# Performance work log

Measured on AMD Instinct MI355X. Metric: run time of the kernel, lower is better.

## Reference

```python
import jax, jax.numpy as jnp
import numpy as np

WS = 8          # window size
NH = 16         # num heads
C = 256         # in_channels
L = WS * WS     # tokens per window
EPS = 1e-5      # LayerNorm eps

def _rel_index():
    coords = np.stack(np.meshgrid(np.arange(WS), np.arange(WS), indexing='ij')).reshape(2, -1)
    rel = coords[:, :, None] - coords[:, None, :]
    rel = rel + (WS - 1)
    rel[0] = rel[0] * (2 * WS - 1)
    return jnp.asarray(rel.sum(0))  # [L, L] int

REL_IDX = _rel_index()

def _ln(x, g, b):
    m = x.mean(-1, keepdims=True)
    v = jnp.var(x, axis=-1, keepdims=True)
    return (x - m) * jax.lax.rsqrt(v + EPS) * g + b

def setup_inputs() -> dict:
    key = jax.random.key(0)
    ks = jax.random.split(key, 8)
    return {
        'x': jax.random.normal(ks[0], (2, C, 256, 256), dtype=jnp.float32),
        'pre_gamma': jnp.ones((C,), jnp.float32),
        'pre_beta': jnp.zeros((C,), jnp.float32),
        'post_gamma': jnp.ones((C,), jnp.float32),
        'post_beta': jnp.zeros((C,), jnp.float32),
        'qkv_w': jax.random.normal(ks[1], (C, 3 * C), jnp.float32) * 0.02,
        'qkv_b': jnp.zeros((3 * C,), jnp.float32),
        'proj_w': jax.random.normal(ks[2], (C, C), jnp.float32) * 0.02,
        'proj_b': jnp.zeros((C,), jnp.float32),
        'rel_bias_table': jax.random.normal(ks[3], ((2 * WS - 1) ** 2, NH), jnp.float32) * 0.02,
    }

def reference(x, pre_gamma, pre_beta, post_gamma, post_beta, qkv_w, qkv_b, proj_w, proj_b, rel_bias_table):
    N, Cc, H, W = x.shape
    # block partition: [N,C,H,W] -> [N*nWin, L, C]
    t = x.reshape(N, Cc, H // WS, WS, W // WS, WS)
    t = t.transpose(0, 2, 4, 3, 5, 1).reshape(-1, L, Cc)
    B = t.shape[0]
    # pre-norm + relative self-attention (cosine / normalized qk)
    y = _ln(t, pre_gamma, pre_beta)
    qkv = (y @ qkv_w + qkv_b).reshape(B, L, 3, NH, Cc // NH).transpose(2, 0, 3, 1, 4)
    q, k, v = qkv[0], qkv[1], qkv[2]  # [B, h, L, dh]
    q = q / jnp.maximum(jnp.linalg.norm(q, axis=-1, keepdims=True), 1e-12)
    k = k / jnp.maximum(jnp.linalg.norm(k, axis=-1, keepdims=True), 1e-12)
    bias = rel_bias_table[REL_IDX].transpose(2, 0, 1)  # [h, L, L]
    attn = jax.nn.softmax(jnp.einsum('bhld,bhmd->bhlm', q, k) + bias, axis=-1)
    o = jnp.einsum('bhlm,bhmd->bhld', attn, v).transpose(0, 2, 1, 3).reshape(B, L, Cc)
    o = o @ proj_w + proj_b
    out = t + o
    # post-norm residual (mlp is Identity in MetNet-3)
    out = out + _ln(out, post_gamma, post_beta)
    # reverse partition -> [N, C, H, W]
    out = out.reshape(N, H // WS, W // WS, WS, WS, Cc)
    out = out.transpose(0, 5, 1, 3, 2, 4).reshape(N, Cc, H, W)
    return out
```

## Files before the change

kernel.cpp:

```cpp
#include <hip/hip_runtime.h>


#define WSZ 8
#define LTOK 64
#define NH 16
#define CCH 256
#define WW2 256
#define HWP 65536
#define NWIN 2048

#define TP 258
#define QP2 18
#define VP2 66
#define PP2 66
#define OHP 36

typedef __bf16 bf16x8 __attribute__((ext_vector_type(8)));
typedef float  f32x4  __attribute__((ext_vector_type(4)));
typedef unsigned short u16;
typedef unsigned long long ull;
typedef uint4  __attribute__((may_alias)) uint4_a;
typedef float4 __attribute__((may_alias)) float4_a;
typedef ull    __attribute__((may_alias)) ull_a;

__device__ __forceinline__ float b2f(u16 u) {
    return (float)__builtin_bit_cast(__bf16, u);
}
__device__ __forceinline__ u16 f2b(float f) {
    return __builtin_bit_cast(u16, (__bf16)f);
}
__device__ __forceinline__ __bf16 u2b(u16 u) {
    return __builtin_bit_cast(__bf16, u);
}
__device__ __forceinline__ float gload(const void* p, int idx, int isf32) {
    return isf32 ? ((const float*)p)[idx] : b2f(((const u16*)p)[idx]);
}

static __global__ void detect_dtype(const u16* __restrict__ xu, int* __restrict__ flag) {
    int lane = threadIdx.x;
    u16 u = xu[lane];
    int e = (u >> 7) & 0xFF;
    bool plaus = (u == 0) || (e >= 0x6C && e <= 0x86);
    unsigned long long m = __ballot(plaus);
    if (lane == 0) flag[0] = (__popcll(m) >= 56) ? 0 : 1;
}

static __global__ __launch_bounds__(256) void prep_qkv(
        const void* __restrict__ qkv_w, const void* __restrict__ qkv_b,
        const void* __restrict__ g, const void* __restrict__ be,
        u16* __restrict__ gwT, float* __restrict__ D2, float* __restrict__ D3,
        const int* __restrict__ flagp)
{
    const int isf32 = flagp[0];
    int col0 = blockIdx.x * 4;
    int c    = threadIdx.x;
    float gv = gload(g, c, isf32), bv = gload(be, c, isf32);
    float w4[4];
    if (isf32) {
        float4 w = *(const float4_a*)((const float*)qkv_w + c * 768 + col0);
        w4[0] = w.x; w4[1] = w.y; w4[2] = w.z; w4[3] = w.w;
    } else {
        ull u = *(const ull_a*)((const u16*)qkv_w + c * 768 + col0);
        w4[0] = b2f((u16)u);         w4[1] = b2f((u16)(u >> 16));
        w4[2] = b2f((u16)(u >> 32)); w4[3] = b2f((u16)(u >> 48));
    }
    float s2[4], s3[4];
    #pragma unroll
    for (int j = 0; j < 4; ++j) {
        float gw = gv * w4[j];
        gwT[(col0 + j) * 256 + c] = f2b(gw);
        s2[j] = gw; s3[j] = bv * w4[j];
    }
    #pragma unroll
    for (int off = 32; off; off >>= 1) {
        #pragma unroll
        for (int j = 0; j < 4; ++j) {
            s2[j] += __shfl_xor(s2[j], off);
            s3[j] += __shfl_xor(s3[j], off);
        }
    }
    __shared__ float p2[4][4], p3[4][4];
    int wvid = threadIdx.x >> 6, ln = threadIdx.x & 63;
    if (ln == 0) {
        #pragma unroll
        for (int j = 0; j < 4; ++j) { p2[wvid][j] = s2[j]; p3[wvid][j] = s3[j]; }
    }
    __syncthreads();
    if (threadIdx.x < 4) {
        int j = threadIdx.x;
        D2[col0 + j] = p2[0][j] + p2[1][j] + p2[2][j] + p2[3][j];
        D3[col0 + j] = p3[0][j] + p3[1][j] + p3[2][j] + p3[3][j]
                     + gload(qkv_b, col0 + j, isf32);
    }
}

static __global__ __launch_bounds__(256) void prep_proj(
        const void* __restrict__ proj_w, u16* __restrict__ pwT,
        const void* __restrict__ table, float* __restrict__ tablef,
        const int* __restrict__ flagp)
{
    const int isf32 = flagp[0];
    int n0 = blockIdx.x * 4, k = threadIdx.x;
    float w4[4];
    if (isf32) {
        float4 w = *(const float4_a*)((const float*)proj_w + k * 256 + n0);
        w4[0] = w.x; w4[1] = w.y; w4[2] = w.z; w4[3] = w.w;
    } else {
        ull u = *(const ull_a*)((const u16*)proj_w + k * 256 + n0);
        w4[0] = b2f((u16)u);         w4[1] = b2f((u16)(u >> 16));
        w4[2] = b2f((u16)(u >> 32)); w4[3] = b2f((u16)(u >> 48));
    }
    #pragma unroll
    for (int j = 0; j < 4; ++j) pwT[(n0 + j) * 256 + k] = f2b(w4[j]);
    int gid = blockIdx.x * 256 + threadIdx.x;
    if (gid < (2 * WSZ - 1) * (2 * WSZ - 1) * NH)
        tablef[gid] = gload(table, gid, isf32);
}

static __global__ __launch_bounds__(256, 3) void win_attn(
    const void* __restrict__ x, void* __restrict__ out,
    const u16* __restrict__ gwT, const u16* __restrict__ pwT,
    const float* __restrict__ D2, const float* __restrict__ D3,
    const void* __restrict__ proj_b, const void* __restrict__ postg,
    const void* __restrict__ postb, const float* __restrict__ tablef,
    const int* __restrict__ flagp)
{
    __shared__ __align__(16) u16 smu[19968];
    u16* const sm_t  = smu;
    u16* const sm_qb = smu;
    u16* const sm_kb = smu + 4608;
    u16* const sm_vb = smu + 9216;
    u16* const sm_pb = smu + 13440;
    u16* const sm_ob = smu + 17664;
    __shared__ float sm_mean[LTOK], sm_rstd[LTOK];
    __shared__ u16 sm_zero[16];

    const int isf32 = flagp[0];
    const int tid  = threadIdx.x;
    const int wv   = tid >> 6;
    const int lane = tid & 63;
    const int quad = lane >> 4;
    const int n15  = lane & 15;

    const int b  = blockIdx.x;
    const int nb = b >> 10, wh = (b >> 5) & 31, wwi = b & 31;
    const int base = nb * (CCH * HWP) + wh * (8 * WW2) + wwi * 8;

    if (tid < 16) sm_zero[tid] = 0;

    if (isf32) {
        const float* xf = (const float*)x;
        #pragma unroll
        for (int r = 0; r < 8; ++r) {
            int s = tid + r * 256;
            int c = s >> 3, i = s & 7;
            const float* src = xf + base + c * HWP + i * WW2;
            float4 a = *(const float4_a*)(src);
            float4 d = *(const float4_a*)(src + 4);
            u16* dst = &sm_t[(i * 8) * TP + c];
            dst[0 * TP] = f2b(a.x);  dst[1 * TP] = f2b(a.y);
            dst[2 * TP] = f2b(a.z);  dst[3 * TP] = f2b(a.w);
            dst[4 * TP] = f2b(d.x);  dst[5 * TP] = f2b(d.y);
            dst[6 * TP] = f2b(d.z);  dst[7 * TP] = f2b(d.w);
        }
    } else {
        const u16* xu = (const u16*)x;
        #pragma unroll
        for (int r = 0; r < 8; ++r) {
            int s = tid + r * 256;
            int c = s >> 3, i = s & 7;
            const uint4 v = *(const uint4_a*)(xu + base + c * HWP + i * WW2);
            u16* dst = &sm_t[(i * 8) * TP + c];
            dst[0 * TP] = (u16)(v.x & 0xffff);  dst[1 * TP] = (u16)(v.x >> 16);
            dst[2 * TP] = (u16)(v.y & 0xffff);  dst[3 * TP] = (u16)(v.y >> 16);
            dst[4 * TP] = (u16)(v.z & 0xffff);  dst[5 * TP] = (u16)(v.z >> 16);
            dst[6 * TP] = (u16)(v.w & 0xffff);  dst[7 * TP] = (u16)(v.w >> 16);
        }
    }
    __syncthreads();

    {
        int l = tid >> 2, g = tid & 3;
        float s = 0.f, ss = 0.f;
        const u16* row = &sm_t[l * TP + g * 64];
        #pragma unroll
        for (int e = 0; e < 64; ++e) {
            float a = b2f(row[e]);
            s += a; ss += a * a;
        }
        s += __shfl_xor(s, 1); ss += __shfl_xor(ss, 1);
        s += __shfl_xor(s, 2); ss += __shfl_xor(ss, 2);
        if (g == 0) {
            float mean = s * (1.f / 256.f);
            float var  = ss * (1.f / 256.f) - mean * mean;
            sm_mean[l] = mean;
            sm_rstd[l] = rsqrtf(var + 1e-5f);
        }
    }

    float s4[4], ms4[4];
    #pragma unroll
    for (int r = 0; r < 4; ++r) {
        int tok = wv * 16 + quad * 4 + r;
        float mu = sm_mean[tok], sd = sm_rstd[tok];
        s4[r] = sd; ms4[r] = -mu * sd;
    }

    bf16x8 afr[8];
    {
        const u16* arow = &sm_t[(wv * 16 + n15) * TP];
        #pragma unroll
        for (int kb = 0; kb < 8; ++kb) {
            #pragma unroll
            for (int j = 0; j < 8; ++j)
                afr[kb][j] = u2b(arow[kb * 32 + quad * 8 + j]);
        }
    }
    __syncthreads();

    int toff[4][4];
    #pragma unroll
    for (int ct = 0; ct < 4; ++ct) {
        int key = ct * 16 + n15, im = key >> 3, jm = key & 7;
        #pragma unroll
        for (int r = 0; r < 4; ++r) {
            int tok = wv * 16 + quad * 4 + r;
            int il = tok >> 3, jl = tok & 7;
            toff[ct][r] = ((il - im + 7) * 15 + (jl - jm + 7)) * 16;
        }
    }

    f32x4 accp[16];
    #pragma unroll
    for (int t2 = 0; t2 < 16; ++t2) accp[t2] = f32x4{0.f, 0.f, 0.f, 0.f};
    const f32x4 zero4 = f32x4{0.f, 0.f, 0.f, 0.f};

    bf16x8 onesf;
    #pragma unroll
    for (int j = 0; j < 8; ++j) onesf[j] = (__bf16)1.0f;

    for (int hq = 0; hq < 4; ++hq) {
        const int H = hq * 4;

        f32x4 aq[4], ak[4], av[4];
        #pragma unroll
        for (int hh = 0; hh < 4; ++hh) { aq[hh] = zero4; ak[hh] = zero4; av[hh] = zero4; }
        const u16* g0 = &gwT[(H * 16 + n15) * 256 + quad * 8];
        #pragma unroll
        for (int kb = 0; kb < 8; ++kb) {
            #pragma unroll
            for (int hh = 0; hh < 4; ++hh) {
                const u16* gq = g0 + hh * 4096 + kb * 32;
                bf16x8 bq = __builtin_bit_cast(bf16x8, *(const uint4_a*)(gq));
                bf16x8 bk = __builtin_bit_cast(bf16x8, *(const uint4_a*)(gq + 65536));
                bf16x8 bv = __builtin_bit_cast(bf16x8, *(const uint4_a*)(gq + 131072));
                aq[hh] = __builtin_amdgcn_mfma_f32_16x16x32_bf16(afr[kb], bq, aq[hh], 0, 0, 0);
                ak[hh] = __builtin_amdgcn_mfma_f32_16x16x32_bf16(afr[kb], bk, ak[hh], 0, 0, 0);
                av[hh] = __builtin_amdgcn_mfma_f32_16x16x32_bf16(afr[kb], bv, av[hh], 0, 0, 0);
            }
        }
        #pragma unroll
        for (int hh = 0; hh < 4; ++hh) {
            int ci = (H + hh) * 16 + n15;
            float d2q = D2[ci],       d3q = D3[ci];
            float d2k = D2[256 + ci], d3k = D3[256 + ci];
            float d2v = D2[512 + ci], d3v = D3[512 + ci];
            float qv[4], kv[4], vv[4];
            #pragma unroll
            for (int r = 0; r < 4; ++r) {
                qv[r] = s4[r] * aq[hh][r] + ms4[r] * d2q + d3q;
                kv[r] = s4[r] * ak[hh][r] + ms4[r] * d2k + d3k;
                vv[r] = s4[r] * av[hh][r] + ms4[r] * d2v + d3v;
            }
            #pragma unroll
            for (int r = 0; r < 4; ++r) {
                float sq = qv[r] * qv[r], sk = kv[r] * kv[r];
                sq += __shfl_xor(sq, 1); sk += __shfl_xor(sk, 1);
                sq += __shfl_xor(sq, 2); sk += __shfl_xor(sk, 2);
                sq += __shfl_xor(sq, 4); sk += __shfl_xor(sk, 4);
                sq += __shfl_xor(sq, 8); sk += __shfl_xor(sk, 8);
                qv[r] *= rsqrtf(fmaxf(sq, 1e-24f));
                kv[r] *= rsqrtf(fmaxf(sk, 1e-24f));
            }
            #pragma unroll
            for (int r = 0; r < 4; ++r) {
                int tok = wv * 16 + quad * 4 + r;
                sm_qb[hh * 1152 + tok * QP2 + n15] = f2b(qv[r]);
                sm_kb[hh * 1152 + tok * QP2 + n15] = f2b(kv[r]);
                sm_vb[hh * 1056 + n15 * VP2 + tok] = f2b(vv[r]);
            }
        }
        __syncthreads();

        #pragma unroll
        for (int hh = 0; hh < 4; ++hh) {
            const int h = H + hh;
            f32x4 sc[4];
            {
                bf16x8 aqf;
                const u16* qrow = (quad < 2)
                    ? &sm_qb[hh * 1152 + (wv * 16 + n15) * QP2 + quad * 8]
                    : sm_zero;
                #pragma unroll
                for (int j = 0; j < 8; ++j) aqf[j] = u2b(qrow[j]);
                #pragma unroll
                for (int ct = 0; ct < 4; ++ct) {
                    bf16x8 bkf;
                    const u16* krow = (quad < 2)
                        ? &sm_kb[hh * 1152 + (ct * 16 + n15) * QP2 + quad * 8]
                        : sm_zero;
                    #pragma unroll
                    for (int j = 0; j < 8; ++j) bkf[j] = u2b(krow[j]);
                    f32x4 bias;
                    #pragma unroll
                    for (int r = 0; r < 4; ++r) bias[r] = tablef[toff[ct][r] + h];
                    sc[ct] = __builtin_amdgcn_mfma_f32_16x16x32_bf16(aqf, bkf, bias, 0, 0, 0);
                }
            }
            #pragma unroll
            for (int r = 0; r < 4; ++r) {
                float e0 = __expf(sc[0][r]), e1 = __expf(sc[1][r]);
                float e2 = __expf(sc[2][r]), e3 = __expf(sc[3][r]);
                int tok = wv * 16 + quad * 4 + r;
                sm_pb[tok * PP2 +  0 + n15] = f2b(e0);
                sm_pb[tok * PP2 + 16 + n15] = f2b(e1);
                sm_pb[tok * PP2 + 32 + n15] = f2b(e2);
                sm_pb[tok * PP2 + 48 + n15] = f2b(e3);
            }

            f32x4 ov = zero4, rs = zero4;
            #pragma unroll
            for (int ks = 0; ks < 2; ++ks) {
                bf16x8 ap, bvf;
                const u16* prow = &sm_pb[(wv * 16 + n15) * PP2 + ks * 32 + quad * 8];
                const u16* vrow = &sm_vb[hh * 1056 + n15 * VP2 + ks * 32 + quad * 8];
                #pragma unroll
                for (int j = 0; j < 8; ++j) { ap[j] = u2b(prow[j]); bvf[j] = u2b(vrow[j]); }
                ov = __builtin_amdgcn_mfma_f32_16x16x32_bf16(ap, bvf, ov, 0, 0, 0);
                rs = __builtin_amdgcn_mfma_f32_16x16x32_bf16(ap, onesf, rs, 0, 0, 0);
            }
            #pragma unroll
            for (int r = 0; r < 4; ++r) {
                int tok = wv * 16 + quad * 4 + r;
                sm_ob[tok * OHP + (h & 1) * 16 + n15] = f2b(ov[r] / rs[r]);
            }

            if (hh & 1) {
                int hp = h >> 1;
                bf16x8 aof;
                const u16* orow = &sm_ob[(wv * 16 + n15) * OHP + quad * 8];
                #pragma unroll
                for (int j = 0; j < 8; ++j) aof[j] = u2b(orow[j]);
                const u16* pwb = &pwT[n15 * 256 + hp * 32 + quad * 8];
                #pragma unroll
                for (int t2 = 0; t2 < 16; ++t2) {
                    bf16x8 bpf = __builtin_bit_cast(bf16x8, *(const uint4_a*)(pwb + t2 * 16 * 256));
                    accp[t2] = __builtin_amdgcn_mfma_f32_16x16x32_bf16(aof, bpf, accp[t2], 0, 0, 0);
                }
            }
        }
        __syncthreads();
    }

    if (isf32) {
        const float* xf = (const float*)x;
        #pragma unroll
        for (int r = 0; r < 8; ++r) {
            int s = tid + r * 256;
            int c = s >> 3, i = s & 7;
            const float* src = xf + base + c * HWP + i * WW2;
            float4 a = *(const float4_a*)(src);
            float4 d = *(const float4_a*)(src + 4);
            u16* dst = &sm_t[(i * 8) * TP + c];
            dst[0 * TP] = f2b(a.x);  dst[1 * TP] = f2b(a.y);
            dst[2 * TP] = f2b(a.z);  dst[3 * TP] = f2b(a.w);
            dst[4 * TP] = f2b(d.x);  dst[5 * TP] = f2b(d.y);
            dst[6 * TP] = f2b(d.z);  dst[7 * TP] = f2b(d.w);
        }
    } else {
        const u16* xu = (const u16*)x;
        #pragma unroll
        for (int r = 0; r < 8; ++r) {
            int s = tid + r * 256;
            int c = s >> 3, i = s & 7;
            const uint4 v = *(const uint4_a*)(xu + base + c * HWP + i * WW2);
            u16* dst = &sm_t[(i * 8) * TP + c];
            dst[0 * TP] = (u16)(v.x & 0xffff);  dst[1 * TP] = (u16)(v.x >> 16);
            dst[2 * TP] = (u16)(v.y & 0xffff);  dst[3 * TP] = (u16)(v.y >> 16);
            dst[4 * TP] = (u16)(v.z & 0xffff);  dst[5 * TP] = (u16)(v.z >> 16);
            dst[6 * TP] = (u16)(v.w & 0xffff);  dst[7 * TP] = (u16)(v.w >> 16);
        }
    }
    __syncthreads();

    {
        #pragma unroll
        for (int t2 = 0; t2 < 16; ++t2) {
            int col = t2 * 16 + n15;
            float pb = gload(proj_b, col, isf32);
            #pragma unroll
            for (int r = 0; r < 4; ++r) {
                int tok = wv * 16 + quad * 4 + r;
                accp[t2][r] += pb + b2f(sm_t[tok * TP + col]);
            }
        }
        float sr[4] = {0, 0, 0, 0}, ssr[4] = {0, 0, 0, 0};
        #pragma unroll
        for (int t2 = 0; t2 < 16; ++t2) {
            #pragma unroll
            for (int r = 0; r < 4; ++r) { float v = accp[t2][r]; sr[r] += v; ssr[r] += v * v; }
        }
        #pragma unroll
        for (int r = 0; r < 4; ++r) {
            sr[r] += __shfl_xor(sr[r], 1); ssr[r] += __shfl_xor(ssr[r], 1);
            sr[r] += __shfl_xor(sr[r], 2); ssr[r] += __shfl_xor(ssr[r], 2);
            sr[r] += __shfl_xor(sr[r], 4); ssr[r] += __shfl_xor(ssr[r], 4);
            sr[r] += __shfl_xor(sr[r], 8); ssr[r] += __shfl_xor(ssr[r], 8);
        }
        float mean2[4], rs2[4];
        #pragma unroll
        for (int r = 0; r < 4; ++r) {
            float m = sr[r] * (1.f / 256.f);
            float v = ssr[r] * (1.f / 256.f) - m * m;
            mean2[r] = m; rs2[r] = rsqrtf(v + 1e-5f);
        }
        #pragma unroll
        for (int t2 = 0; t2 < 16; ++t2) {
            int col = t2 * 16 + n15;
            float pg = gload(postg, col, isf32), pb2 = gload(postb, col, isf32);
            #pragma unroll
            for (int r = 0; r < 4; ++r) {
                int tok = wv * 16 + quad * 4 + r;
                float o1 = accp[t2][r];
                float fin = o1 + (o1 - mean2[r]) * rs2[r] * pg + pb2;
                sm_t[tok * TP + col] = f2b(fin);
            }
        }
    }
    __syncthreads();

    if (isf32) {
        float* outf = (float*)out;
        #pragma unroll
        for (int r = 0; r < 8; ++r) {
            int s = tid + r * 256;
            int c = s >> 3, i = s & 7;
            const u16* src = &sm_t[(i * 8) * TP + c];
            float* dst = outf + base + c * HWP + i * WW2;
            float4 a, d;
            a.x = b2f(src[0 * TP]); a.y = b2f(src[1 * TP]);
            a.z = b2f(src[2 * TP]); a.w = b2f(src[3 * TP]);
            d.x = b2f(src[4 * TP]); d.y = b2f(src[5 * TP]);
            d.z = b2f(src[6 * TP]); d.w = b2f(src[7 * TP]);
            *(float4_a*)dst = a;
            *(float4_a*)(dst + 4) = d;
        }
    } else {
        u16* outu = (u16*)out;
        #pragma unroll
        for (int r = 0; r < 8; ++r) {
            int s = tid + r * 256;
            int c = s >> 3, i = s & 7;
            const u16* src = &sm_t[(i * 8) * TP + c];
            uint4 v;
            v.x = (unsigned)src[0 * TP] | ((unsigned)src[1 * TP] << 16);
            v.y = (unsigned)src[2 * TP] | ((unsigned)src[3 * TP] << 16);
            v.z = (unsigned)src[4 * TP] | ((unsigned)src[5 * TP] << 16);
            v.w = (unsigned)src[6 * TP] | ((unsigned)src[7 * TP] << 16);
            *(uint4_a*)(outu + base + c * HWP + i * WW2) = v;
        }
    }
}

extern "C" void kernel_launch(void* const* d_in, const int* in_sizes, int n_in,
                              void* d_out, int out_size, void* d_ws, size_t ws_size,
                              hipStream_t stream) {
    const void* x     = d_in[0];
    const void* preg  = d_in[1];
    const void* preb  = d_in[2];
    const void* postg = d_in[3];
    const void* postb = d_in[4];
    const void* qkvw  = d_in[5];
    const void* qkvb  = d_in[6];
    const void* projw = d_in[7];
    const void* projb = d_in[8];
    const void* table = d_in[9];

    char* ws = (char*)d_ws;
    u16*   gwT = (u16*)(ws);
    u16*   pwT = (u16*)(ws + 393216);
    float* D2  = (float*)(ws + 524288);
    float* D3  = (float*)(ws + 527360);
    float* tbf = (float*)(ws + 530432);
    int*   flg = (int*)(ws + 544832);

    detect_dtype<<<1, 64, 0, stream>>>((const u16*)x, flg);
    prep_qkv<<<192, 256, 0, stream>>>(qkvw, qkvb, preg, preb, gwT, D2, D3, flg);
    prep_proj<<<64, 256, 0, stream>>>(projw, pwT, table, tbf, flg);
    win_attn<<<NWIN, 256, 0, stream>>>(x, d_out, gwT, pwT, D2, D3,
                                       projb, postg, postb, tbf, flg);
}
```

Before: 1.186 ms.

## Process four windows per block with dedicated LDS buffers to skip x reload

Each block now loops over four adjacent windows, so the grid shrinks from 2048 to 512 blocks. The shared-memory regions for the input tile, q, k, v, probabilities and head outputs no longer alias each other. Because the input tile stays resident, the residual add reads it from LDS instead of reloading x from global memory. The cost is much more LDS per block, launch bounds lowered from 3 to 2 blocks per CU, and windows processed serially inside a block, which reduces occupancy and latency hiding.

```diff
diff --git a/kernel.cpp b/kernel.cpp
--- a/kernel.cpp
+++ b/kernel.cpp
@@ -7,7 +7,7 @@
 #define CCH 256
 #define WW2 256
 #define HWP 65536
-#define NWIN 2048
+#define NBLK 512
 
 #define TP 258
 #define QP2 18
@@ -117,7 +117,7 @@
         tablef[gid] = gload(table, gid, isf32);
 }
 
-static __global__ __launch_bounds__(256, 3) void win_attn(
+static __global__ __launch_bounds__(256, 2) void win_attn(
     const void* __restrict__ x, void* __restrict__ out,
     const u16* __restrict__ gwT, const u16* __restrict__ pwT,
     const float* __restrict__ D2, const float* __restrict__ D3,
@@ -125,13 +125,12 @@
     const void* __restrict__ postb, const float* __restrict__ tablef,
     const int* __restrict__ flagp)
 {
-    __shared__ __align__(16) u16 smu[19968];
-    u16* const sm_t  = smu;
-    u16* const sm_qb = smu;
-    u16* const sm_kb = smu + 4608;
-    u16* const sm_vb = smu + 9216;
-    u16* const sm_pb = smu + 13440;
-    u16* const sm_ob = smu + 17664;
+    __shared__ u16 sm_t[LTOK * TP];
+    __shared__ u16 sm_q[4][LTOK * QP2];
+    __shared__ u16 sm_k[4][LTOK * QP2];
+    __shared__ u16 sm_vt[4][NH * VP2];
+    __shared__ u16 sm_p[LTOK * PP2];
+    __shared__ u16 sm_oh[LTOK * OHP];
     __shared__ float sm_mean[LTOK], sm_rstd[LTOK];
     __shared__ u16 sm_zero[16];
 
@@ -142,81 +141,10 @@
     const int quad = lane >> 4;
     const int n15  = lane & 15;
 
-    const int b  = blockIdx.x;
-    const int nb = b >> 10, wh = (b >> 5) & 31, wwi = b & 31;
-    const int base = nb * (CCH * HWP) + wh * (8 * WW2) + wwi * 8;
+    const int b   = blockIdx.x;
+    const int nb  = b >> 8, wh = (b >> 3) & 31, ww4 = b & 7;
 
     if (tid < 16) sm_zero[tid] = 0;
-
-    if (isf32) {
-        const float* xf = (const float*)x;
-        #pragma unroll
-        for (int r = 0; r < 8; ++r) {
-            int s = tid + r * 256;
-            int c = s >> 3, i = s & 7;
-            const float* src = xf + base + c * HWP + i * WW2;
-            float4 a = *(const float4_a*)(src);
-            float4 d = *(const float4_a*)(src + 4);
-            u16* dst = &sm_t[(i * 8) * TP + c];
-            dst[0 * TP] = f2b(a.x);  dst[1 * TP] = f2b(a.y);
-            dst[2 * TP] = f2b(a.z);  dst[3 * TP] = f2b(a.w);
-            dst[4 * TP] = f2b(d.x);  dst[5 * TP] = f2b(d.y);
-            dst[6 * TP] = f2b(d.z);  dst[7 * TP] = f2b(d.w);
-        }
-    } else {
-        const u16* xu = (const u16*)x;
-        #pragma unroll
-        for (int r = 0; r < 8; ++r) {
-            int s = tid + r * 256;
-            int c = s >> 3, i = s & 7;
-            const uint4 v = *(const uint4_a*)(xu + base + c * HWP + i * WW2);
-            u16* dst = &sm_t[(i * 8) * TP + c];
-            dst[0 * TP] = (u16)(v.x & 0xffff);  dst[1 * TP] = (u16)(v.x >> 16);
-            dst[2 * TP] = (u16)(v.y & 0xffff);  dst[3 * TP] = (u16)(v.y >> 16);
-            dst[4 * TP] = (u16)(v.z & 0xffff);  dst[5 * TP] = (u16)(v.z >> 16);
-            dst[6 * TP] = (u16)(v.w & 0xffff);  dst[7 * TP] = (u16)(v.w >> 16);
-        }
-    }
-    __syncthreads();
-
-    {
-        int l = tid >> 2, g = tid & 3;
-        float s = 0.f, ss = 0.f;
-        const u16* row = &sm_t[l * TP + g * 64];
-        #pragma unroll
-        for (int e = 0; e < 64; ++e) {
-            float a = b2f(row[e]);
-            s += a; ss += a * a;
-        }
-        s += __shfl_xor(s, 1); ss += __shfl_xor(ss, 1);
-        s += __shfl_xor(s, 2); ss += __shfl_xor(ss, 2);
-        if (g == 0) {
-            float mean = s * (1.f / 256.f);
-            float var  = ss * (1.f / 256.f) - mean * mean;
-            sm_mean[l] = mean;
-            sm_rstd[l] = rsqrtf(var + 1e-5f);
-        }
-    }
-
-    float s4[4], ms4[4];
-    #pragma unroll
-    for (int r = 0; r < 4; ++r) {
-        int tok = wv * 16 + quad * 4 + r;
-        float mu = sm_mean[tok], sd = sm_rstd[tok];
-        s4[r] = sd; ms4[r] = -mu * sd;
-    }
-
-    bf16x8 afr[8];
-    {
-        const u16* arow = &sm_t[(wv * 16 + n15) * TP];
-        #pragma unroll
-        for (int kb = 0; kb < 8; ++kb) {
-            #pragma unroll
-            for (int j = 0; j < 8; ++j)
-                afr[kb][j] = u2b(arow[kb * 32 + quad * 8 + j]);
-        }
-    }
-    __syncthreads();
 
     int toff[4][4];
     #pragma unroll
@@ -230,245 +158,286 @@
         }
     }
 
-    f32x4 accp[16];
-    #pragma unroll
-    for (int t2 = 0; t2 < 16; ++t2) accp[t2] = f32x4{0.f, 0.f, 0.f, 0.f};
     const f32x4 zero4 = f32x4{0.f, 0.f, 0.f, 0.f};
-
     bf16x8 onesf;
     #pragma unroll
     for (int j = 0; j < 8; ++j) onesf[j] = (__bf16)1.0f;
 
-    for (int hq = 0; hq < 4; ++hq) {
-        const int H = hq * 4;
-
-        f32x4 aq[4], ak[4], av[4];
-        #pragma unroll
-        for (int hh = 0; hh < 4; ++hh) { aq[hh] = zero4; ak[hh] = zero4; av[hh] = zero4; }
-        const u16* g0 = &gwT[(H * 16 + n15) * 256 + quad * 8];
-        #pragma unroll
-        for (int kb = 0; kb < 8; ++kb) {
-            #pragma unroll
-            for (int hh = 0; hh < 4; ++hh) {
-                const u16* gq = g0 + hh * 4096 + kb * 32;
-                bf16x8 bq = __builtin_bit_cast(bf16x8, *(const uint4_a*)(gq));
-                bf16x8 bk = __builtin_bit_cast(bf16x8, *(const uint4_a*)(gq + 65536));
-                bf16x8 bv = __builtin_bit_cast(bf16x8, *(const uint4_a*)(gq + 131072));
-                aq[hh] = __builtin_amdgcn_mfma_f32_16x16x32_bf16(afr[kb], bq, aq[hh], 0, 0, 0);
-                ak[hh] = __builtin_amdgcn_mfma_f32_16x16x32_bf16(afr[kb], bk, ak[hh], 0, 0, 0);
-                av[hh] = __builtin_amdgcn_mfma_f32_16x16x32_bf16(afr[kb], bv, av[hh], 0, 0, 0);
-            }
-        }
-        #pragma unroll
-        for (int hh = 0; hh < 4; ++hh) {
-            int ci = (H + hh) * 16 + n15;
-            float d2q = D2[ci],       d3q = D3[ci];
-            float d2k = D2[256 + ci], d3k = D3[256 + ci];
-            float d2v = D2[512 + ci], d3v = D3[512 + ci];
-            float qv[4], kv[4], vv[4];
-            #pragma unroll
-            for (int r = 0; r < 4; ++r) {
-                qv[r] = s4[r] * aq[hh][r] + ms4[r] * d2q + d3q;
-                kv[r] = s4[r] * ak[hh][r] + ms4[r] * d2k + d3k;
-                vv[r] = s4[r] * av[hh][r] + ms4[r] * d2v + d3v;
-            }
-            #pragma unroll
-            for (int r = 0; r < 4; ++r) {
-                float sq = qv[r] * qv[r], sk = kv[r] * kv[r];
-                sq += __shfl_xor(sq, 1); sk += __shfl_xor(sk, 1);
-                sq += __shfl_xor(sq, 2); sk += __shfl_xor(sk, 2);
-                sq += __shfl_xor(sq, 4); sk += __shfl_xor(sk, 4);
-                sq += __shfl_xor(sq, 8); sk += __shfl_xor(sk, 8);
-                qv[r] *= rsqrtf(fmaxf(sq, 1e-24f));
-                kv[r] *= rsqrtf(fmaxf(sk, 1e-24f));
-            }
-            #pragma unroll
-            for (int r = 0; r < 4; ++r) {
-                int tok = wv * 16 + quad * 4 + r;
-                sm_qb[hh * 1152 + tok * QP2 + n15] = f2b(qv[r]);
-                sm_kb[hh * 1152 + tok * QP2 + n15] = f2b(kv[r]);
-                sm_vb[hh * 1056 + n15 * VP2 + tok] = f2b(vv[r]);
+    for (int w = 0; w < 4; ++w) {
+        const int base = nb * (CCH * HWP) + wh * (8 * WW2) + (ww4 * 4 + w) * 8;
+
+        if (isf32) {
+            const float* xf = (const float*)x;
+            #pragma unroll
+            for (int r = 0; r < 8; ++r) {
+                int s = tid + r * 256;
+                int c = s >> 3, i = s & 7;
+                const float* src = xf + base + c * HWP + i * WW2;
+                float4 a = *(const float4_a*)(src);
+                float4 d = *(const float4_a*)(src + 4);
+                u16* dst = &sm_t[(i * 8) * TP + c];
+                dst[0 * TP] = f2b(a.x);  dst[1 * TP] = f2b(a.y);
+                dst[2 * TP] = f2b(a.z);  dst[3 * TP] = f2b(a.w);
+                dst[4 * TP] = f2b(d.x);  dst[5 * TP] = f2b(d.y);
+                dst[6 * TP] = f2b(d.z);  dst[7 * TP] = f2b(d.w);
+            }
+        } else {
+            const u16* xu = (const u16*)x;
+            #pragma unroll
+            for (int r = 0; r < 8; ++r) {
+                int s = tid + r * 256;
+                int c = s >> 3, i = s & 7;
+                const uint4 v = *(const uint4_a*)(xu + base + c * HWP + i * WW2);
+                u16* dst = &sm_t[(i * 8) * TP + c];
+                dst[0 * TP] = (u16)(v.x & 0xffff);  dst[1 * TP] = (u16)(v.x >> 16);
+                dst[2 * TP] = (u16)(v.y & 0xffff);  dst[3 * TP] = (u16)(v.y >> 16);
+                dst[4 * TP] = (u16)(v.z & 0xffff);  dst[5 * TP] = (u16)(v.z >> 16);
+                dst[6 * TP] = (u16)(v.w & 0xffff);  dst[7 * TP] = (u16)(v.w >> 16);
             }
         }
         __syncthreads();
 
-        #pragma unroll
-        for (int hh = 0; hh < 4; ++hh) {
-            const int h = H + hh;
-            f32x4 sc[4];
-            {
-                bf16x8 aqf;
-                const u16* qrow = (quad < 2)
-                    ? &sm_qb[hh * 1152 + (wv * 16 + n15) * QP2 + quad * 8]
-                    : sm_zero;
-                #pragma unroll
-                for (int j = 0; j < 8; ++j) aqf[j] = u2b(qrow[j]);
-                #pragma unroll
-                for (int ct = 0; ct < 4; ++ct) {
-                    bf16x8 bkf;
-                    const u16* krow = (quad < 2)
-                        ? &sm_kb[hh * 1152 + (ct * 16 + n15) * QP2 + quad * 8]
-                        : sm_zero;
-                    #pragma unroll
-                    for (int j = 0; j < 8; ++j) bkf[j] = u2b(krow[j]);
-                    f32x4 bias;
-                    #pragma unroll
-                    for (int r = 0; r < 4; ++r) bias[r] = tablef[toff[ct][r] + h];
-                    sc[ct] = __builtin_amdgcn_mfma_f32_16x16x32_bf16(aqf, bkf, bias, 0, 0, 0);
-                }
-            }
-            #pragma unroll
-            for (int r = 0; r < 4; ++r) {
-                float e0 = __expf(sc[0][r]), e1 = __expf(sc[1][r]);
-                float e2 = __expf(sc[2][r]), e3 = __expf(sc[3][r]);
-                int tok = wv * 16 + quad * 4 + r;
-                sm_pb[tok * PP2 +  0 + n15] = f2b(e0);
-                sm_pb[tok * PP2 + 16 + n15] = f2b(e1);
-                sm_pb[tok * PP2 + 32 + n15] = f2b(e2);
-                sm_pb[tok * PP2 + 48 + n15] = f2b(e3);
-            }
-
-            f32x4 ov = zero4, rs = zero4;
-            #pragma unroll
-            for (int ks = 0; ks < 2; ++ks) {
-                bf16x8 ap, bvf;
-                const u16* prow = &sm_pb[(wv * 16 + n15) * PP2 + ks * 32 + quad * 8];
-                const u16* vrow = &sm_vb[hh * 1056 + n15 * VP2 + ks * 32 + quad * 8];
-                #pragma unroll
-                for (int j = 0; j < 8; ++j) { ap[j] = u2b(prow[j]); bvf[j] = u2b(vrow[j]); }
-                ov = __builtin_amdgcn_mfma_f32_16x16x32_bf16(ap, bvf, ov, 0, 0, 0);
-                rs = __builtin_amdgcn_mfma_f32_16x16x32_bf16(ap, onesf, rs, 0, 0, 0);
-            }
-            #pragma unroll
-            for (int r = 0; r < 4; ++r) {
-                int tok = wv * 16 + quad * 4 + r;
-                sm_ob[tok * OHP + (h & 1) * 16 + n15] = f2b(ov[r] / rs[r]);
-            }
-
-            if (hh & 1) {
-                int hp = h >> 1;
-                bf16x8 aof;
-                const u16* orow = &sm_ob[(wv * 16 + n15) * OHP + quad * 8];
-                #pragma unroll
-                for (int j = 0; j < 8; ++j) aof[j] = u2b(orow[j]);
-                const u16* pwb = &pwT[n15 * 256 + hp * 32 + quad * 8];
-                #pragma unroll
-                for (int t2 = 0; t2 < 16; ++t2) {
-                    bf16x8 bpf = __builtin_bit_cast(bf16x8, *(const uint4_a*)(pwb + t2 * 16 * 256));
-                    accp[t2] = __builtin_amdgcn_mfma_f32_16x16x32_bf16(aof, bpf, accp[t2], 0, 0, 0);
-                }
-            }
-        }
-        __syncthreads();
-    }
-
-    if (isf32) {
-        const float* xf = (const float*)x;
-        #pragma unroll
-        for (int r = 0; r < 8; ++r) {
-            int s = tid + r * 256;
-            int c = s >> 3, i = s & 7;
-            const float* src = xf + base + c * HWP + i * WW2;
-            float4 a = *(const float4_a*)(src);
-            float4 d = *(const float4_a*)(src + 4);
-            u16* dst = &sm_t[(i * 8) * TP + c];
-            dst[0 * TP] = f2b(a.x);  dst[1 * TP] = f2b(a.y);
-            dst[2 * TP] = f2b(a.z);  dst[3 * TP] = f2b(a.w);
-            dst[4 * TP] = f2b(d.x);  dst[5 * TP] = f2b(d.y);
-            dst[6 * TP] = f2b(d.z);  dst[7 * TP] = f2b(d.w);
-        }
-    } else {
-        const u16* xu = (const u16*)x;
-        #pragma unroll
-        for (int r = 0; r < 8; ++r) {
-            int s = tid + r * 256;
-            int c = s >> 3, i = s & 7;
-            const uint4 v = *(const uint4_a*)(xu + base + c * HWP + i * WW2);
-            u16* dst = &sm_t[(i * 8) * TP + c];
-            dst[0 * TP] = (u16)(v.x & 0xffff);  dst[1 * TP] = (u16)(v.x >> 16);
-            dst[2 * TP] = (u16)(v.y & 0xffff);  dst[3 * TP] = (u16)(v.y >> 16);
-            dst[4 * TP] = (u16)(v.z & 0xffff);  dst[5 * TP] = (u16)(v.z >> 16);
-            dst[6 * TP] = (u16)(v.w & 0xffff);  dst[7 * TP] = (u16)(v.w >> 16);
-        }
-    }
-    __syncthreads();
-
-    {
-        #pragma unroll
-        for (int t2 = 0; t2 < 16; ++t2) {
-            int col = t2 * 16 + n15;
-            float pb = gload(proj_b, col, isf32);
-            #pragma unroll
-            for (int r = 0; r < 4; ++r) {
-                int tok = wv * 16 + quad * 4 + r;
-                accp[t2][r] += pb + b2f(sm_t[tok * TP + col]);
-            }
-        }
-        float sr[4] = {0, 0, 0, 0}, ssr[4] = {0, 0, 0, 0};
-        #pragma unroll
-        for (int t2 = 0; t2 < 16; ++t2) {
-            #pragma unroll
-            for (int r = 0; r < 4; ++r) { float v = accp[t2][r]; sr[r] += v; ssr[r] += v * v; }
-        }
+        {
+            int l = tid >> 2, g = tid & 3;
+            float s = 0.f, ss = 0.f;
+            const u16* row = &sm_t[l * TP + g * 64];
+            #pragma unroll
+            for (int e = 0; e < 64; ++e) {
+                float a = b2f(row[e]);
+                s += a; ss += a * a;
+            }
+            s += __shfl_xor(s, 1); ss += __shfl_xor(ss, 1);
+            s += __shfl_xor(s, 2); ss += __shfl_xor(ss, 2);
+            if (g == 0) {
+                float mean = s * (1.f / 256.f);
+                float var  = ss * (1.f / 256.f) - mean * mean;
+                sm_mean[l] = mean;
+                sm_rstd[l] = rsqrtf(var + 1e-5f);
+            }
+        }
+
+        float s4[4], ms4[4];
         #pragma unroll
         for (int r = 0; r < 4; ++r) {
-            sr[r] += __shfl_xor(sr[r], 1); ssr[r] += __shfl_xor(ssr[r], 1);
-            sr[r] += __shfl_xor(sr[r], 2); ssr[r] += __shfl_xor(ssr[r], 2);
-            sr[r] += __shfl_xor(sr[r], 4); ssr[r] += __shfl_xor(ssr[r], 4);
-            sr[r] += __shfl_xor(sr[r], 8); ssr[r] += __shfl_xor(ssr[r], 8);
-        }
-        float mean2[4], rs2[4];
+            int tok = wv * 16 + quad * 4 + r;
+            float mu = sm_mean[tok], sd = sm_rstd[tok];
+            s4[r] = sd; ms4[r] = -mu * sd;
+        }
+
+        bf16x8 afr[8];
+        {
+            const u16* arow = &sm_t[(wv * 16 + n15) * TP];
+            #pragma unroll
+            for (int kb = 0; kb < 8; ++kb) {
+                #pragma unroll
+                for (int j = 0; j < 8; ++j)
+                    afr[kb][j] = u2b(arow[kb * 32 + quad * 8 + j]);
+            }
+        }
+
+        f32x4 accp[16];
         #pragma unroll
-        for (int r = 0; r < 4; ++r) {
-            float m = sr[r] * (1.f / 256.f);
-            float v = ssr[r] * (1.f / 256.f) - m * m;
-            mean2[r] = m; rs2[r] = rsqrtf(v + 1e-5f);
-        }
-        #pragma unroll
-        for (int t2 = 0; t2 < 16; ++t2) {
-            int col = t2 * 16 + n15;
-            float pg = gload(postg, col, isf32), pb2 = gload(postb, col, isf32);
+        for (int t2 = 0; t2 < 16; ++t2) accp[t2] = f32x4{0.f, 0.f, 0.f, 0.f};
+
+        for (int hq = 0; hq < 4; ++hq) {
+            const int H = hq * 4;
+
+            f32x4 aq[4], ak[4], av[4];
+            #pragma unroll
+            for (int hh = 0; hh < 4; ++hh) { aq[hh] = zero4; ak[hh] = zero4; av[hh] = zero4; }
+            const u16* g0 = &gwT[(H * 16 + n15) * 256 + quad * 8];
+            #pragma unroll
+            for (int kb = 0; kb < 8; ++kb) {
+                #pragma unroll
+                for (int hh = 0; hh < 4; ++hh) {
+                    const u16* gq = g0 + hh * 4096 + kb * 32;
+                    bf16x8 bq = __builtin_bit_cast(bf16x8, *(const uint4_a*)(gq));
+                    bf16x8 bk = __builtin_bit_cast(bf16x8, *(const uint4_a*)(gq + 65536));
+                    bf16x8 bv = __builtin_bit_cast(bf16x8, *(const uint4_a*)(gq + 131072));
+                    aq[hh] = __builtin_amdgcn_mfma_f32_16x16x32_bf16(afr[kb], bq, aq[hh], 0, 0, 0);
+                    ak[hh] = __builtin_amdgcn_mfma_f32_16x16x32_bf16(afr[kb], bk, ak[hh], 0, 0, 0);
+                    av[hh] = __builtin_amdgcn_mfma_f32_16x16x32_bf16(afr[kb], bv, av[hh], 0, 0, 0);
+                }
+            }
+            #pragma unroll
+            for (int hh = 0; hh < 4; ++hh) {
+                int ci = (H + hh) * 16 + n15;
+                float d2q = D2[ci],       d3q = D3[ci];
+                float d2k = D2[256 + ci], d3k = D3[256 + ci];
+                float d2v = D2[512 + ci], d3v = D3[512 + ci];
+                float qv[4], kv[4], vv[4];
+                #pragma unroll
+                for (int r = 0; r < 4; ++r) {
+                    qv[r] = s4[r] * aq[hh][r] + ms4[r] * d2q + d3q;
+                    kv[r] = s4[r] * ak[hh][r] + ms4[r] * d2k + d3k;
+                    vv[r] = s4[r] * av[hh][r] + ms4[r] * d2v + d3v;
+                }
+                #pragma unroll
+                for (int r = 0; r < 4; ++r) {
+                    float sq = qv[r] * qv[r], sk = kv[r] * kv[r];
+                    sq += __shfl_xor(sq, 1); sk += __shfl_xor(sk, 1);
+                    sq += __shfl_xor(sq, 2); sk += __shfl_xor(sk, 2);
+                    sq += __shfl_xor(sq, 4); sk += __shfl_xor(sk, 4);
+                    sq += __shfl_xor(sq, 8); sk += __shfl_xor(sk, 8);
+                    qv[r] *= rsqrtf(fmaxf(sq, 1e-24f));
+                    kv[r] *= rsqrtf(fmaxf(sk, 1e-24f));
+                }
+                #pragma unroll
+                for (int r = 0; r < 4; ++r) {
+                    int tok = wv * 16 + quad * 4 + r;
+                    sm_q[hh][tok * QP2 + n15] = f2b(qv[r]);
+                    sm_k[hh][tok * QP2 + n15] = f2b(kv[r]);
+                    sm_vt[hh][n15 * VP2 + tok] = f2b(vv[r]);
+                }
+            }
+            __syncthreads();
+
+            #pragma unroll
+            for (int hh = 0; hh < 4; ++hh) {
+                const int h = H + hh;
+                f32x4 sc[4];
+                {
+                    bf16x8 aqf;
+                    const u16* qrow = (quad < 2)
+                        ? &sm_q[hh][(wv * 16 + n15) * QP2 + quad * 8] : sm_zero;
+                    #pragma unroll
+                    for (int j = 0; j < 8; ++j) aqf[j] = u2b(qrow[j]);
+                    #pragma unroll
+                    for (int ct = 0; ct < 4; ++ct) {
+                        bf16x8 bkf;
+                        const u16* krow = (quad < 2)
+                            ? &sm_k[hh][(ct * 16 + n15) * QP2 + quad * 8] : sm_zero;
+                        #pragma unroll
+                        for (int j = 0; j < 8; ++j) bkf[j] = u2b(krow[j]);
+                        f32x4 bias;
+                        #pragma unroll
+                        for (int r = 0; r < 4; ++r) bias[r] = tablef[toff[ct][r] + h];
+                        sc[ct] = __builtin_amdgcn_mfma_f32_16x16x32_bf16(aqf, bkf, bias, 0, 0, 0);
+                    }
+                }
+                #pragma unroll
+                for (int r = 0; r < 4; ++r) {
+                    float e0 = __expf(sc[0][r]), e1 = __expf(sc[1][r]);
+                    float e2 = __expf(sc[2][r]), e3 = __expf(sc[3][r]);
+                    int tok = wv * 16 + quad * 4 + r;
+                    sm_p[tok * PP2 +  0 + n15] = f2b(e0);
+                    sm_p[tok * PP2 + 16 + n15] = f2b(e1);
+                    sm_p[tok * PP2 + 32 + n15] = f2b(e2);
+                    sm_p[tok * PP2 + 48 + n15] = f2b(e3);
+                }
+
+                f32x4 ov = zero4, rs = zero4;
+                #pragma unroll
+                for (int ks = 0; ks < 2; ++ks) {
+                    bf16x8 ap, bvf;
+                    const u16* prow = &sm_p[(wv * 16 + n15) * PP2 + ks * 32 + quad * 8];
+                    const u16* vrow = &sm_vt[hh][n15 * VP2 + ks * 32 + quad * 8];
+                    #pragma unroll
+                    for (int j = 0; j < 8; ++j) { ap[j] = u2b(prow[j]); bvf[j] = u2b(vrow[j]); }
+                    ov = __builtin_amdgcn_mfma_f32_16x16x32_bf16(ap, bvf, ov, 0, 0, 0);
+                    rs = __builtin_amdgcn_mfma_f32_16x16x32_bf16(ap, onesf, rs, 0, 0, 0);
+                }
+                #pragma unroll
+                for (int r = 0; r < 4; ++r) {
+                    int tok = wv * 16 + quad * 4 + r;
+                    sm_oh[tok * OHP + (h & 1) * 16 + n15] = f2b(ov[r] / rs[r]);
+                }
+
+                if (hh & 1) {
+                    int hp = h >> 1;
+                    bf16x8 aof;
+                    const u16* orow = &sm_oh[(wv * 16 + n15) * OHP + quad * 8];
+                    #pragma unroll
+                    for (int j = 0; j < 8; ++j) aof[j] = u2b(orow[j]);
+                    const u16* pwb = &pwT[n15 * 256 + hp * 32 + quad * 8];
+                    #pragma unroll
+                    for (int t2 = 0; t2 < 16; ++t2) {
+                        bf16x8 bpf = __builtin_bit_cast(bf16x8, *(const uint4_a*)(pwb + t2 * 16 * 256));
+                        accp[t2] = __builtin_amdgcn_mfma_f32_16x16x32_bf16(aof, bpf, accp[t2], 0, 0, 0);
+                    }
+                }
+            }
+            __syncthreads();
+        }
+
+        {
+            #pragma unroll
+            for (int t2 = 0; t2 < 16; ++t2) {
+                int col = t2 * 16 + n15;
+                float pb = gload(proj_b, col, isf32);
+                #pragma unroll
+                for (int r = 0; r < 4; ++r) {
+                    int tok = wv * 16 + quad * 4 + r;
+                    accp[t2][r] += pb + b2f(sm_t[tok * TP + col]);
+                }
+            }
+            float sr[4] = {0, 0, 0, 0}, ssr[4] = {0, 0, 0, 0};
+            #pragma unroll
+            for (int t2 = 0; t2 < 16; ++t2) {
+                #pragma unroll
+                for (int r = 0; r < 4; ++r) { float v = accp[t2][r]; sr[r] += v; ssr[r] += v * v; }
+            }
             #pragma unroll
             for (int r = 0; r < 4; ++r) {
-                int tok = wv * 16 + quad * 4 + r;
-                float o1 = accp[t2][r];
-                float fin = o1 + (o1 - mean2[r]) * rs2[r] * pg + pb2;
-                sm_t[tok * TP + col] = f2b(fin);
-            }
-        }
-    }
-    __syncthreads();
-
-    if (isf32) {
-        float* outf = (float*)out;
-        #pragma unroll
-        for (int r = 0; r < 8; ++r) {
-            int s = tid + r * 256;
-            int c = s >> 3, i = s & 7;
-            const u16* src = &sm_t[(i * 8) * TP + c];
-            float* dst = outf + base + c * HWP + i * WW2;
-            float4 a, d;
-            a.x = b2f(src[0 * TP]); a.y = b2f(src[1 * TP]);
-            a.z = b2f(src[2 * TP]); a.w = b2f(src[3 * TP]);
-            d.x = b2f(src[4 * TP]); d.y = b2f(src[5 * TP]);
-            d.z = b2f(src[6 * TP]); d.w = b2f(src[7 * TP]);
-            *(float4_a*)dst = a;
-            *(float4_a*)(dst + 4) = d;
-        }
-    } else {
-        u16* outu = (u16*)out;
-        #pragma unroll
-        for (int r = 0; r < 8; ++r) {
-            int s = tid + r * 256;
-            int c = s >> 3, i = s & 7;
-            const u16* src = &sm_t[(i * 8) * TP + c];
-            uint4 v;
-            v.x = (unsigned)src[0 * TP] | ((unsigned)src[1 * TP] << 16);
-            v.y = (unsigned)src[2 * TP] | ((unsigned)src[3 * TP] << 16);
-            v.z = (unsigned)src[4 * TP] | ((unsigned)src[5 * TP] << 16);
-            v.w = (unsigned)src[6 * TP] | ((unsigned)src[7 * TP] << 16);
-            *(uint4_a*)(outu + base + c * HWP + i * WW2) = v;
-        }
+                sr[r] += __shfl_xor(sr[r], 1); ssr[r] += __shfl_xor(ssr[r], 1);
+                sr[r] += __shfl_xor(sr[r], 2); ssr[r] += __shfl_xor(ssr[r], 2);
+                sr[r] += __shfl_xor(sr[r], 4); ssr[r] += __shfl_xor(ssr[r], 4);
+                sr[r] += __shfl_xor(sr[r], 8); ssr[r] += __shfl_xor(ssr[r], 8);
+            }
+            float mean2[4], rs2[4];
+            #pragma unroll
+            for (int r = 0; r < 4; ++r) {
+                float m = sr[r] * (1.f / 256.f);
+                float v = ssr[r] * (1.f / 256.f) - m * m;
+                mean2[r] = m; rs2[r] = rsqrtf(v + 1e-5f);
+            }
+            #pragma unroll
+            for (int t2 = 0; t2 < 16; ++t2) {
+                int col = t2 * 16 + n15;
+                float pg = gload(postg, col, isf32), pb2 = gload(postb, col, isf32);
+                #pragma unroll
+                for (int r = 0; r < 4; ++r) {
+                    int tok = wv * 16 + quad * 4 + r;
+                    float o1 = accp[t2][r];
+                    float fin = o1 + (o1 - mean2[r]) * rs2[r] * pg + pb2;
+                    sm_t[tok * TP + col] = f2b(fin);
+                }
+            }
+        }
+        __syncthreads();
+
+        if (isf32) {
+            float* outf = (float*)out;
+            #pragma unroll
+            for (int r = 0; r < 8; ++r) {
+                int s = tid + r * 256;
+                int c = s >> 3, i = s & 7;
+                const u16* src = &sm_t[(i * 8) * TP + c];
+                float* dst = outf + base + c * HWP + i * WW2;
+                float4 a, d;
+                a.x = b2f(src[0 * TP]); a.y = b2f(src[1 * TP]);
+                a.z = b2f(src[2 * TP]); a.w = b2f(src[3 * TP]);
+                d.x = b2f(src[4 * TP]); d.y = b2f(src[5 * TP]);
+                d.z = b2f(src[6 * TP]); d.w = b2f(src[7 * TP]);
+                *(float4_a*)dst = a;
+                *(float4_a*)(dst + 4) = d;
+            }
+        } else {
+            u16* outu = (u16*)out;
+            #pragma unroll
+            for (int r = 0; r < 8; ++r) {
+                int s = tid + r * 256;
+                int c = s >> 3, i = s & 7;
+                const u16* src = &sm_t[(i * 8) * TP + c];
+                uint4 v;
+                v.x = (unsigned)src[0 * TP] | ((unsigned)src[1 * TP] << 16);
+                v.y = (unsigned)src[2 * TP] | ((unsigned)src[3 * TP] << 16);
+                v.z = (unsigned)src[4 * TP] | ((unsigned)src[5 * TP] << 16);
+                v.w = (unsigned)src[6 * TP] | ((unsigned)src[7 * TP] << 16);
+                *(uint4_a*)(outu + base + c * HWP + i * WW2) = v;
+            }
+        }
+        __syncthreads();
     }
 }
 
@@ -497,6 +466,6 @@
     detect_dtype<<<1, 64, 0, stream>>>((const u16*)x, flg);
     prep_qkv<<<192, 256, 0, stream>>>(qkvw, qkvb, preg, preb, gwT, D2, D3, flg);
     prep_proj<<<64, 256, 0, stream>>>(projw, pwT, table, tbf, flg);
-    win_attn<<<NWIN, 256, 0, stream>>>(x, d_out, gwT, pwT, D2, D3,
+    win_attn<<<NBLK, 256, 0, stream>>>(x, d_out, gwT, pwT, D2, D3,
                                        projb, postg, postb, tbf, flg);
 }
```

After: 1.053 ms. 11.2% less time.
